# Kernel optimization log

Hardware: AMD Instinct MI355X
Metric: run time of the kernel (lower is better)

Reference implementation:

```python
import jax, jax.numpy as jnp
import numpy as np

DPITCH_RANGE = 24.0
SCALE = 1.0

B, T, ND, SD, H = 8192, 256, 8, 3, 64
HIST = 64
L = T - HIST  # generated LSTM steps; L+1 outputs emitted
IN = ND + SD + 1


def setup_inputs() -> dict:
    key = jax.random.key(0)
    ks = jax.random.split(key, 11)
    s = 1.0 / np.sqrt(H)

    def u(k, shape):
        return jax.random.uniform(k, shape, jnp.float32, -s, s)

    return {
        "noise": jax.random.normal(ks[0], (B, T, ND), jnp.float32),
        "hist_x": jax.random.normal(ks[1], (B, HIST, SD), jnp.float32) * 0.1,
        "gap_duration": jax.random.uniform(ks[2], (B, L + 1, SD - 1), jnp.float32),
        "W_ih": u(ks[3], (4 * H, IN)),
        "W_hh": u(ks[4], (4 * H, H)),
        "b_ih": u(ks[5], (4 * H,)),
        "b_hh": u(ks[6], (4 * H,)),
        "W1": u(ks[7], (H, H)),
        "b1": u(ks[8], (H,)),
        "W2": u(ks[9], (1, H)),
        "b2": u(ks[10], (1,)),
    }


def reference(noise, hist_x, gap_duration, W_ih, W_hh, b_ih, b_hh, W1, b1, W2, b2):
    hist_len = hist_x.shape[1]
    bias = b_ih + b_hh

    def lstm_cell(x, h, c):
        # PyTorch gate order: i, f, g, o
        gates = x @ W_ih.T + h @ W_hh.T + bias
        i, f, g, o = jnp.split(gates, 4, axis=-1)
        c = jax.nn.sigmoid(f) * c + jax.nn.sigmoid(i) * jnp.tanh(g)
        h = jax.nn.sigmoid(o) * jnp.tanh(c)
        return h, c

    # ---- conditioning on history ----
    dist = jnp.cumsum(hist_x[:, :, -1:], axis=1)                 # [B,HIST,1]
    cond_in = jnp.concatenate([hist_x, dist, noise[:, :hist_len]], axis=-1)  # [B,HIST,IN]
    h0 = jnp.zeros((noise.shape[0], W_hh.shape[1]), noise.dtype)
    c0 = jnp.zeros_like(h0)

    def cond_step(carry, x_t):
        h, c = carry
        h, c = lstm_cell(x_t, h, c)
        return (h, c), None

    (h, c), _ = jax.lax.scan(cond_step, (h0, c0), jnp.swapaxes(cond_in, 0, 1))
    output = h                      # last LSTM output [B,H]
    dist = dist[:, -1, :]           # [B,1]

    gen_noise = noise[:, hist_len:]                               # [B,L,ND]
    # pad one zero step: the final LSTM update is computed but unused
    gen_noise = jnp.concatenate(
        [gen_noise, jnp.zeros((gen_noise.shape[0], 1, gen_noise.shape[2]), gen_noise.dtype)], axis=1)
    xs = (jnp.swapaxes(gap_duration, 0, 1), jnp.swapaxes(gen_noise, 0, 1))

    def gen_step(carry, x_t):
        h, c, out, dist = carry
        gd, nz = x_t
        z = jnp.tanh(jnp.tanh(out @ W1.T + b1) @ W2.T + b2)       # output_net
        dp = z * DPITCH_RANGE * SCALE                             # [B,1]
        x = jnp.concatenate([gd, dp], axis=-1)                    # [B,SD]
        dist = dist + dp
        inp = jnp.concatenate([x, dist, nz], axis=-1)             # [B,IN]
        h, c = lstm_cell(inp, h, c)
        return (h, c, h, dist), x

    _, gen_xs = jax.lax.scan(gen_step, (h, c, output, dist), xs)  # [L+1,B,SD]
    output_seq = jnp.swapaxes(gen_xs, 0, 1)                       # [B,L+1,SD]
    return jnp.concatenate([hist_x, output_seq], axis=1)          # [B,HIST+L+1,SD]
```

## Files before the change

### kernel.cpp

```cpp
#include <hip/hip_runtime.h>
#include <stdint.h>

typedef unsigned short u16;
typedef unsigned int u32;
typedef __attribute__((ext_vector_type(8))) short short8v;
typedef __attribute__((ext_vector_type(4))) float f32x4;

#define NB 16
#define HISTN 64
#define TGEN 193

#define S_NOISE 2048
#define S_HIST  192
#define S_GAP   386
#define S_OUT   771

#define HROW 104
#define L2E  1.442695041f
#define L2E2 2.885390082f

__device__ __forceinline__ float b2f(u16 u) { return __uint_as_float(((u32)u) << 16); }
__device__ __forceinline__ u16 f2b(float f) {
    u32 u = __float_as_uint(f);
    u32 r = (u + 0x7fffu + ((u >> 16) & 1u)) >> 16;
    return (u16)r;
}
__device__ __forceinline__ float rcp_(float x) { return __builtin_amdgcn_rcpf(x); }
__device__ __forceinline__ float ex2(float x) { return __builtin_amdgcn_exp2f(x); }
__device__ __forceinline__ u32 cvtpk(float a, float b) {
    u32 r; asm("v_cvt_pk_bf16_f32 %0, %1, %2" : "=v"(r) : "v"(a), "v"(b)); return r;
}
__device__ __forceinline__ float tanh2(float s) {
    return __builtin_fmaf(-2.0f, rcp_(1.0f + ex2(s)), 1.0f);
}
__device__ __forceinline__ float cellh(const f32x4 a, float& c) {
    float iv = rcp_(1.0f + ex2(a[0]));
    float fv = rcp_(1.0f + ex2(a[1]));
    float gv = tanh2(a[2]);
    float ov = rcp_(1.0f + ex2(a[3]));
    c = __builtin_fmaf(fv, c, iv * gv);
    return ov * tanh2(L2E2 * c);
}
__device__ __forceinline__ float ldv(const void* p, int idx, bool f32) {
    return f32 ? ((const float*)p)[idx] : b2f(((const u16*)p)[idx]);
}
__device__ __forceinline__ void sync_lds() {
    asm volatile("s_waitcnt lgkmcnt(0)" ::: "memory");
    __builtin_amdgcn_s_barrier();
}

extern "C" __global__ void __launch_bounds__(512, 4)
lstm_gen_kernel(const void* __restrict__ noise, const void* __restrict__ hist_x,
                const void* __restrict__ gap, const void* __restrict__ pW_ih,
                const void* __restrict__ pW_hh, const void* __restrict__ pb_ih,
                const void* __restrict__ pb_hh, const void* __restrict__ pW1,
                const void* __restrict__ pb1, const void* __restrict__ pW2,
                const void* __restrict__ pb2, void* __restrict__ out)
{
    __shared__ u16 hb[2][NB * HROW];
    __shared__ u16 cxsA[HISTN][NB][8];
    __shared__ u16 cxsB[HISTN][NB][8];
    __shared__ u32 gdsb[TGEN * NB];
    __shared__ u16 nring[32][NB][8];
    __shared__ float zpl[NB * 4];
    __shared__ float dpd[NB];

    const int tid = threadIdx.x;
    const int lane = tid & 63;
    const int w = tid >> 6;
    const int lg = lane >> 4;
    const int ln = lane & 15;

    bool is_f32 = false;
    {
        const u32* p = (const u32*)pW_hh;
        for (int i = 0; i < 64; i++) {
            u32 v = p[i];
            float a = b2f((u16)(v & 0xffffu));
            float bb = b2f((u16)(v >> 16));
            if (!(fabsf(a) <= 0.5f) || !(fabsf(bb) <= 0.5f)) is_f32 = true;
        }
    }

    float* hs = (float*)gdsb;

    for (int i = tid; i < NB * HROW; i += 512) ((u32*)hb)[i] = 0u;
    for (int i = tid; i < HISTN * NB * 3; i += 512) {
        int t = i / 48, r = i % 48, b = r / 3, k = r % 3;
        hs[i] = ldv(hist_x, ((size_t)blockIdx.x * NB + b) * S_HIST + t * 3 + k, is_f32);
    }
    for (int i = tid; i < HISTN * NB * 4; i += 512) {
        int t = i >> 6, r = i & 63, b = r >> 2, q = r & 3;
        size_t base = ((size_t)blockIdx.x * NB + b) * S_NOISE + t * 8;
        u32 v;
        if (is_f32) {
            const float* p = (const float*)noise + base + q * 2;
            v = (u32)f2b(p[0]) | ((u32)f2b(p[1]) << 16);
        } else v = ((const u32*)noise)[(base >> 1) + q];
        ((u32*)&cxsB[t][b][0])[q] = v;
    }
    {
        const int s = tid >> 4, b = tid & 15;
        size_t base = ((size_t)blockIdx.x * NB + b) * S_NOISE + (size_t)(HISTN + s) * 8;
        u32 r0, r1, r2, r3;
        if (is_f32) {
            const float* nf = (const float*)noise + base;
            float4 a = *(const float4*)nf, bq = *(const float4*)(nf + 4);
            r0 = (u32)f2b(a.x) | ((u32)f2b(a.y) << 16);
            r1 = (u32)f2b(a.z) | ((u32)f2b(a.w) << 16);
            r2 = (u32)f2b(bq.x) | ((u32)f2b(bq.y) << 16);
            r3 = (u32)f2b(bq.z) | ((u32)f2b(bq.w) << 16);
        } else {
            uint4 nv = *(const uint4*)((const u16*)noise + base);
            r0 = nv.x; r1 = nv.y; r2 = nv.z; r3 = nv.w;
        }
        u32* dst = (u32*)&nring[s][b][0];
        dst[0] = r0; dst[1] = r1; dst[2] = r2; dst[3] = r3;
    }
    for (int i = tid; i < NB * HISTN * 3; i += 512) {
        int b = i / 192, e = i % 192;
        size_t bt = (size_t)blockIdx.x * NB + b;
        if (is_f32) ((float*)out)[bt * S_OUT + e] = ((const float*)hist_x)[bt * S_HIST + e];
        else ((u16*)out)[bt * S_OUT + e] = ((const u16*)hist_x)[bt * S_HIST + e];
    }
    __syncthreads();

    if (tid < NB) {
        float dd = 0.0f;
#pragma unroll 1
        for (int t = 0; t < HISTN; t++) {
            float x0 = hs[t * 48 + tid * 3 + 0];
            float x1 = hs[t * 48 + tid * 3 + 1];
            float x2 = hs[t * 48 + tid * 3 + 2];
            dd += x2;
            u16 dph = f2b(x2); u16 dpl = f2b(x2 - b2f(dph));
            u16 dsh = f2b(dd); u16 dsl = f2b(dd - b2f(dsh));
            u32* dst = (u32*)&cxsA[t][tid][0];
            dst[0] = (u32)f2b(x0) | ((u32)f2b(x1) << 16);
            dst[1] = (u32)dph | ((u32)dpl << 16);
            dst[2] = (u32)dsh | ((u32)dsl << 16);
            dst[3] = (u32)dsh | ((u32)dph << 16);
        }
        dpd[tid] = dd;
    }
    __syncthreads();

    for (int i = tid; i < TGEN * NB; i += 512) {
        int t = i >> 4, b = i & 15;
        size_t base = ((size_t)blockIdx.x * NB + b) * S_GAP + t * 2;
        u32 v;
        if (is_f32) {
            const float* p = (const float*)gap + base;
            v = (u32)f2b(p[0]) | ((u32)f2b(p[1]) << 16);
        } else v = *(const u32*)((const u16*)gap + base);
        gdsb[i] = v;
    }

    short8v a00, a01, a02, a10, a11, a12;
#pragma unroll
    for (int T = 0; T < 2; T++) {
        const int j = (T << 5) | (w << 2) | (ln >> 2);
        const int g = ln & 3;
        const int row = (g << 6) | j;
        const float rs = (g == 2) ? L2E2 : -L2E;
        float wdp = ldv(pW_ih, row * 12 + 2, is_f32) * rs;
        u16 wdph = f2b(wdp); u16 wdpl = f2b(wdp - b2f(wdph));
        float wds = ldv(pW_ih, row * 12 + 3, is_f32) * rs;
        u16 wdsh = f2b(wds); u16 wdsl = f2b(wds - b2f(wdsh));
        short8v f0, f1, f2;
#pragma unroll
        for (int e = 0; e < 8; e++) {
            const int c = lg * 8 + e;
            f0[e] = (short)f2b(ldv(pW_hh, row * 64 + c, is_f32) * rs);
            f1[e] = (short)f2b(ldv(pW_hh, row * 64 + 32 + c, is_f32) * rs);
            u16 v = 0;
            if (c == 0 || c == 1) v = f2b(ldv(pW_ih, row * 12 + c, is_f32) * rs);
            else if (c == 2 || c == 3) v = wdph;
            else if (c == 4 || c == 5) v = wdsh;
            else if (c == 6) v = wdsl;
            else if (c == 7) v = wdpl;
            else if (c >= 8 && c < 16) v = f2b(ldv(pW_ih, row * 12 + (c - 4), is_f32) * rs);
            f2[e] = (short)v;
        }
        if (T == 0) { a00 = f0; a01 = f1; a02 = f2; }
        else        { a10 = f0; a11 = f1; a12 = f2; }
    }

    f32x4 bias0, bias1, wd0, wd1, ws0, ws1;
#pragma unroll
    for (int T = 0; T < 2; T++) {
        const int jc = (T << 5) | (w << 2) | lg;
        f32x4 bv, dv, sv;
#pragma unroll
        for (int q = 0; q < 4; q++) {
            const int row = (q << 6) | jc;
            const float qs = (q == 2) ? L2E2 : -L2E;
            bv[q] = (ldv(pb_ih, row, is_f32) + ldv(pb_hh, row, is_f32)) * qs;
            dv[q] = ldv(pW_ih, row * 12 + 2, is_f32) * qs;
            sv[q] = ldv(pW_ih, row * 12 + 3, is_f32) * qs;
        }
        if (T == 0) { bias0 = bv; wd0 = dv; ws0 = sv; }
        else        { bias1 = bv; wd1 = dv; ws1 = sv; }
    }

    const bool mlpw = (w >= 4);
    short8v w1F0 = {}, w1F1 = {};
    f32x4 b1v = {0.f, 0.f, 0.f, 0.f};
    float w2L[4] = {0.f, 0.f, 0.f, 0.f};
    if (mlpw) {
        const int wp = w - 4;
        const int row1 = (wp << 4) | ln;
#pragma unroll
        for (int e = 0; e < 8; e++) {
            w1F0[e] = (short)f2b(ldv(pW1, row1 * 64 + lg * 8 + e, is_f32) * L2E2);
            w1F1[e] = (short)f2b(ldv(pW1, row1 * 64 + 32 + lg * 8 + e, is_f32) * L2E2);
        }
        const int rq = (wp << 4) | (lg << 2);
#pragma unroll
        for (int q = 0; q < 4; q++) {
            b1v[q] = ldv(pb1, rq + q, is_f32) * L2E2;
            w2L[q] = ldv(pW2, rq + q, is_f32) * L2E2;
        }
    }
    const float b2vs = ldv(pb2, 0, is_f32) * L2E2;

    const size_t gb = (size_t)blockIdx.x * NB + (size_t)ln;
    const float* gd_f = (const float*)gap + gb * S_GAP;
    u16* out_h = (u16*)out + gb * S_OUT;
    float* out_f = (float*)out + gb * S_OUT;

    float cst0 = 0.f, cst1 = 0.f;
    int pc = 0;
    __syncthreads();

#pragma unroll 1
    for (int t = 0; t < HISTN; t++) {
        const u16* hc = hb[pc];
        u16* hn = hb[pc ^ 1];
        short8v bf0 = *(const short8v*)&hc[ln * HROW + lg * 8];
        short8v bf1 = *(const short8v*)&hc[ln * HROW + 32 + lg * 8];
        short8v bf2 = {};
        if (lg == 0) bf2 = *(const short8v*)&cxsA[t][ln][0];
        else if (lg == 1) bf2 = *(const short8v*)&cxsB[t][ln][0];
        f32x4 acc0 = bias0, acc1 = bias1;
        acc0 = __builtin_amdgcn_mfma_f32_16x16x32_bf16(a00, bf0, acc0, 0, 0, 0);
        acc0 = __builtin_amdgcn_mfma_f32_16x16x32_bf16(a01, bf1, acc0, 0, 0, 0);
        acc0 = __builtin_amdgcn_mfma_f32_16x16x32_bf16(a02, bf2, acc0, 0, 0, 0);
        acc1 = __builtin_amdgcn_mfma_f32_16x16x32_bf16(a10, bf0, acc1, 0, 0, 0);
        acc1 = __builtin_amdgcn_mfma_f32_16x16x32_bf16(a11, bf1, acc1, 0, 0, 0);
        acc1 = __builtin_amdgcn_mfma_f32_16x16x32_bf16(a12, bf2, acc1, 0, 0, 0);
        float h0 = cellh(acc0, cst0);
        float h1 = cellh(acc1, cst1);
        u32 hp = cvtpk(h0, h1);
        const int j0 = (w << 2) | lg;
        hn[ln * HROW + j0] = (u16)hp;
        hn[ln * HROW + j0 + 32] = (u16)(hp >> 16);
        sync_lds();
        pc ^= 1;
    }

    float dist = dpd[ln];
    float gdf0 = 0.f, gdf1 = 0.f;
    if (is_f32 && tid < NB) { gdf0 = gd_f[0]; gdf1 = gd_f[1]; }

#pragma unroll 1
    for (int tg = 0; tg < TGEN; tg++) {
        u16* hB = hb[0];
        short8v bf0 = *(const short8v*)&hB[ln * HROW + lg * 8];
        short8v bf1 = *(const short8v*)&hB[ln * HROW + 32 + lg * 8];
        short8v bf2 = {};
        u32 g32 = 0;
        if (lg == 0) {
            g32 = gdsb[(tg << 4) | ln];
            bf2[0] = (short)(g32 & 0xffffu); bf2[1] = (short)(g32 >> 16);
        } else if (lg == 1) {
            union { uint4 u; short8v s; } cvt;
            cvt.u = *(const uint4*)&nring[tg & 31][ln][0];
            bf2 = cvt.s;
        }
        f32x4 acc0 = bias0, acc1 = bias1;
        acc0 = __builtin_amdgcn_mfma_f32_16x16x32_bf16(a00, bf0, acc0, 0, 0, 0);
        acc0 = __builtin_amdgcn_mfma_f32_16x16x32_bf16(a01, bf1, acc0, 0, 0, 0);
        acc0 = __builtin_amdgcn_mfma_f32_16x16x32_bf16(a02, bf2, acc0, 0, 0, 0);
        acc1 = __builtin_amdgcn_mfma_f32_16x16x32_bf16(a10, bf0, acc1, 0, 0, 0);
        acc1 = __builtin_amdgcn_mfma_f32_16x16x32_bf16(a11, bf1, acc1, 0, 0, 0);
        acc1 = __builtin_amdgcn_mfma_f32_16x16x32_bf16(a12, bf2, acc1, 0, 0, 0);
        if (mlpw) {
            f32x4 m0 = b1v;
            m0 = __builtin_amdgcn_mfma_f32_16x16x32_bf16(w1F0, bf0, m0, 0, 0, 0);
            m0 = __builtin_amdgcn_mfma_f32_16x16x32_bf16(w1F1, bf1, m0, 0, 0, 0);
            float mp = w2L[0] * tanh2(m0[0]) + w2L[1] * tanh2(m0[1])
                     + w2L[2] * tanh2(m0[2]) + w2L[3] * tanh2(m0[3]);
            mp += __shfl_xor(mp, 16);
            mp += __shfl_xor(mp, 32);
            if (lg == 0) zpl[(ln << 2) | (w - 4)] = mp;
        }
        if (((tg & 15) == 0) && tg > 0 && tg <= 176 && tid < 256) {
            const int s = tid >> 4, b = tid & 15;
            const int t = HISTN + tg + 16 + s;
            u32 r0 = 0, r1 = 0, r2 = 0, r3 = 0;
            if (t < 256) {
                size_t base = ((size_t)blockIdx.x * NB + b) * S_NOISE + (size_t)t * 8;
                if (is_f32) {
                    const float* nf = (const float*)noise + base;
                    float4 a = *(const float4*)nf, bq = *(const float4*)(nf + 4);
                    r0 = (u32)f2b(a.x) | ((u32)f2b(a.y) << 16);
                    r1 = (u32)f2b(a.z) | ((u32)f2b(a.w) << 16);
                    r2 = (u32)f2b(bq.x) | ((u32)f2b(bq.y) << 16);
                    r3 = (u32)f2b(bq.z) | ((u32)f2b(bq.w) << 16);
                } else {
                    uint4 nv = *(const uint4*)((const u16*)noise + base);
                    r0 = nv.x; r1 = nv.y; r2 = nv.z; r3 = nv.w;
                }
            }
            u32* dst = (u32*)&nring[(tg + 16 + s) & 31][b][0];
            dst[0] = r0; dst[1] = r1; dst[2] = r2; dst[3] = r3;
        }
        sync_lds();
        f32x4 zr = *(const f32x4*)&zpl[ln << 2];
        float th = tanh2(b2vs + zr[0] + zr[1] + zr[2] + zr[3]);
        float dp = 24.0f * th;
        dist += dp;
#pragma unroll
        for (int q = 0; q < 4; q++) {
            acc0[q] += wd0[q] * dp + ws0[q] * dist;
            acc1[q] += wd1[q] * dp + ws1[q] * dist;
        }
        float h0 = cellh(acc0, cst0);
        float h1 = cellh(acc1, cst1);
        u32 hp = cvtpk(h0, h1);
        const int j0 = (w << 2) | lg;
        hB[ln * HROW + j0] = (u16)hp;
        hB[ln * HROW + j0 + 32] = (u16)(hp >> 16);
        if (tid < NB) {
            const int to = HISTN + tg;
            if (is_f32) {
                out_f[to * 3] = gdf0; out_f[to * 3 + 1] = gdf1; out_f[to * 3 + 2] = dp;
                if (tg + 1 < TGEN) { gdf0 = gd_f[(tg + 1) * 2]; gdf1 = gd_f[(tg + 1) * 2 + 1]; }
            } else {
                out_h[to * 3] = (u16)(g32 & 0xffffu);
                out_h[to * 3 + 1] = (u16)(g32 >> 16);
                out_h[to * 3 + 2] = f2b(dp);
            }
        }
        sync_lds();
    }
}

extern "C" void kernel_launch(void* const* d_in, const int* in_sizes, int n_in,
                              void* d_out, int out_size, void* d_ws, size_t ws_size,
                              hipStream_t stream) {
    (void)in_sizes; (void)n_in; (void)d_ws; (void)ws_size; (void)out_size;
    lstm_gen_kernel<<<512, 512, 0, stream>>>(
        d_in[0], d_in[1], d_in[2], d_in[3], d_in[4], d_in[5],
        d_in[6], d_in[7], d_in[8], d_in[9], d_in[10], d_out);
}
```

Baseline: 435.8 us.

## Interleave hidden units per lane and merge input buffers into unified LDS rows

Each lane's two hidden units become adjacent (u = w*8 + lg*2 + T), so the packed bf16 pair is written with one 32-bit LDS store instead of two 16-bit stores. The separate cond-phase input buffers and the gap/noise buffers are merged into single 16-element-per-batch rows, so the extra MFMA operand is one 16-byte LDS load instead of branchy partial loads. Gap values now stream through the same 32-slot ring as noise instead of being staged in full, which shrinks LDS use. The dp/dist correction is also written as explicit FMAs.

```diff
diff --git a/kernel.cpp b/kernel.cpp
--- a/kernel.cpp
+++ b/kernel.cpp
@@ -58,10 +58,8 @@
                 const void* __restrict__ pb2, void* __restrict__ out)
 {
     __shared__ u16 hb[2][NB * HROW];
-    __shared__ u16 cxsA[HISTN][NB][8];
-    __shared__ u16 cxsB[HISTN][NB][8];
-    __shared__ u32 gdsb[TGEN * NB];
-    __shared__ u16 nring[32][NB][8];
+    __shared__ u16 cxs[HISTN][NB][16];
+    __shared__ u16 xr[32][NB][16];
     __shared__ float zpl[NB * 4];
     __shared__ float dpd[NB];
 
@@ -82,7 +80,7 @@
         }
     }
 
-    float* hs = (float*)gdsb;
+    float* hs = (float*)xr;
 
     for (int i = tid; i < NB * HROW; i += 512) ((u32*)hb)[i] = 0u;
     for (int i = tid; i < HISTN * NB * 3; i += 512) {
@@ -97,25 +95,7 @@
             const float* p = (const float*)noise + base + q * 2;
             v = (u32)f2b(p[0]) | ((u32)f2b(p[1]) << 16);
         } else v = ((const u32*)noise)[(base >> 1) + q];
-        ((u32*)&cxsB[t][b][0])[q] = v;
-    }
-    {
-        const int s = tid >> 4, b = tid & 15;
-        size_t base = ((size_t)blockIdx.x * NB + b) * S_NOISE + (size_t)(HISTN + s) * 8;
-        u32 r0, r1, r2, r3;
-        if (is_f32) {
-            const float* nf = (const float*)noise + base;
-            float4 a = *(const float4*)nf, bq = *(const float4*)(nf + 4);
-            r0 = (u32)f2b(a.x) | ((u32)f2b(a.y) << 16);
-            r1 = (u32)f2b(a.z) | ((u32)f2b(a.w) << 16);
-            r2 = (u32)f2b(bq.x) | ((u32)f2b(bq.y) << 16);
-            r3 = (u32)f2b(bq.z) | ((u32)f2b(bq.w) << 16);
-        } else {
-            uint4 nv = *(const uint4*)((const u16*)noise + base);
-            r0 = nv.x; r1 = nv.y; r2 = nv.z; r3 = nv.w;
-        }
-        u32* dst = (u32*)&nring[s][b][0];
-        dst[0] = r0; dst[1] = r1; dst[2] = r2; dst[3] = r3;
+        ((u32*)&cxs[t][b][8])[q] = v;
     }
     for (int i = tid; i < NB * HISTN * 3; i += 512) {
         int b = i / 192, e = i % 192;
@@ -135,7 +115,7 @@
             dd += x2;
             u16 dph = f2b(x2); u16 dpl = f2b(x2 - b2f(dph));
             u16 dsh = f2b(dd); u16 dsl = f2b(dd - b2f(dsh));
-            u32* dst = (u32*)&cxsA[t][tid][0];
+            u32* dst = (u32*)&cxs[t][tid][0];
             dst[0] = (u32)f2b(x0) | ((u32)f2b(x1) << 16);
             dst[1] = (u32)dph | ((u32)dpl << 16);
             dst[2] = (u32)dsh | ((u32)dsl << 16);
@@ -145,23 +125,38 @@
     }
     __syncthreads();
 
-    for (int i = tid; i < TGEN * NB; i += 512) {
-        int t = i >> 4, b = i & 15;
-        size_t base = ((size_t)blockIdx.x * NB + b) * S_GAP + t * 2;
-        u32 v;
+    {
+        const int s = tid >> 4, b = tid & 15;
+        u32* row = (u32*)&xr[s][b][0];
+        size_t gbase = ((size_t)blockIdx.x * NB + b) * S_GAP + s * 2;
+        u32 gv;
         if (is_f32) {
-            const float* p = (const float*)gap + base;
-            v = (u32)f2b(p[0]) | ((u32)f2b(p[1]) << 16);
-        } else v = *(const u32*)((const u16*)gap + base);
-        gdsb[i] = v;
+            const float* p = (const float*)gap + gbase;
+            gv = (u32)f2b(p[0]) | ((u32)f2b(p[1]) << 16);
+        } else gv = *(const u32*)((const u16*)gap + gbase);
+        row[0] = gv; row[1] = 0u; row[2] = 0u; row[3] = 0u;
+        size_t nbase = ((size_t)blockIdx.x * NB + b) * S_NOISE + (size_t)(HISTN + s) * 8;
+        u32 r0, r1, r2, r3;
+        if (is_f32) {
+            const float* nf = (const float*)noise + nbase;
+            float4 a = *(const float4*)nf, bq = *(const float4*)(nf + 4);
+            r0 = (u32)f2b(a.x) | ((u32)f2b(a.y) << 16);
+            r1 = (u32)f2b(a.z) | ((u32)f2b(a.w) << 16);
+            r2 = (u32)f2b(bq.x) | ((u32)f2b(bq.y) << 16);
+            r3 = (u32)f2b(bq.z) | ((u32)f2b(bq.w) << 16);
+        } else {
+            uint4 nv = *(const uint4*)((const u16*)noise + nbase);
+            r0 = nv.x; r1 = nv.y; r2 = nv.z; r3 = nv.w;
+        }
+        row[4] = r0; row[5] = r1; row[6] = r2; row[7] = r3;
     }
 
     short8v a00, a01, a02, a10, a11, a12;
 #pragma unroll
     for (int T = 0; T < 2; T++) {
-        const int j = (T << 5) | (w << 2) | (ln >> 2);
+        const int u = (w << 3) | ((ln >> 2) << 1) | T;
         const int g = ln & 3;
-        const int row = (g << 6) | j;
+        const int row = (g << 6) | u;
         const float rs = (g == 2) ? L2E2 : -L2E;
         float wdp = ldv(pW_ih, row * 12 + 2, is_f32) * rs;
         u16 wdph = f2b(wdp); u16 wdpl = f2b(wdp - b2f(wdph));
@@ -189,11 +184,11 @@
     f32x4 bias0, bias1, wd0, wd1, ws0, ws1;
 #pragma unroll
     for (int T = 0; T < 2; T++) {
-        const int jc = (T << 5) | (w << 2) | lg;
+        const int u = (w << 3) | (lg << 1) | T;
         f32x4 bv, dv, sv;
 #pragma unroll
         for (int q = 0; q < 4; q++) {
-            const int row = (q << 6) | jc;
+            const int row = (q << 6) | u;
             const float qs = (q == 2) ? L2E2 : -L2E;
             bv[q] = (ldv(pb_ih, row, is_f32) + ldv(pb_hh, row, is_f32)) * qs;
             dv[q] = ldv(pW_ih, row * 12 + 2, is_f32) * qs;
@@ -231,6 +226,7 @@
 
     float cst0 = 0.f, cst1 = 0.f;
     int pc = 0;
+    const int hoff = (w << 3) | (lg << 1);
     __syncthreads();
 
 #pragma unroll 1
@@ -240,8 +236,7 @@
         short8v bf0 = *(const short8v*)&hc[ln * HROW + lg * 8];
         short8v bf1 = *(const short8v*)&hc[ln * HROW + 32 + lg * 8];
         short8v bf2 = {};
-        if (lg == 0) bf2 = *(const short8v*)&cxsA[t][ln][0];
-        else if (lg == 1) bf2 = *(const short8v*)&cxsB[t][ln][0];
+        if (lg < 2) bf2 = *(const short8v*)&cxs[t][ln][lg * 8];
         f32x4 acc0 = bias0, acc1 = bias1;
         acc0 = __builtin_amdgcn_mfma_f32_16x16x32_bf16(a00, bf0, acc0, 0, 0, 0);
         acc0 = __builtin_amdgcn_mfma_f32_16x16x32_bf16(a01, bf1, acc0, 0, 0, 0);
@@ -251,10 +246,7 @@
         acc1 = __builtin_amdgcn_mfma_f32_16x16x32_bf16(a12, bf2, acc1, 0, 0, 0);
         float h0 = cellh(acc0, cst0);
         float h1 = cellh(acc1, cst1);
-        u32 hp = cvtpk(h0, h1);
-        const int j0 = (w << 2) | lg;
-        hn[ln * HROW + j0] = (u16)hp;
-        hn[ln * HROW + j0 + 32] = (u16)(hp >> 16);
+        *(u32*)&hn[ln * HROW + hoff] = cvtpk(h0, h1);
         sync_lds();
         pc ^= 1;
     }
@@ -269,15 +261,7 @@
         short8v bf0 = *(const short8v*)&hB[ln * HROW + lg * 8];
         short8v bf1 = *(const short8v*)&hB[ln * HROW + 32 + lg * 8];
         short8v bf2 = {};
-        u32 g32 = 0;
-        if (lg == 0) {
-            g32 = gdsb[(tg << 4) | ln];
-            bf2[0] = (short)(g32 & 0xffffu); bf2[1] = (short)(g32 >> 16);
-        } else if (lg == 1) {
-            union { uint4 u; short8v s; } cvt;
-            cvt.u = *(const uint4*)&nring[tg & 31][ln][0];
-            bf2 = cvt.s;
-        }
+        if (lg < 2) bf2 = *(const short8v*)&xr[tg & 31][ln][lg * 8];
         f32x4 acc0 = bias0, acc1 = bias1;
         acc0 = __builtin_amdgcn_mfma_f32_16x16x32_bf16(a00, bf0, acc0, 0, 0, 0);
         acc0 = __builtin_amdgcn_mfma_f32_16x16x32_bf16(a01, bf1, acc0, 0, 0, 0);
@@ -297,24 +281,33 @@
         }
         if (((tg & 15) == 0) && tg > 0 && tg <= 176 && tid < 256) {
             const int s = tid >> 4, b = tid & 15;
-            const int t = HISTN + tg + 16 + s;
+            const int tga = tg + 16 + s;
+            u32* row = (u32*)&xr[tga & 31][b][0];
+            u32 gv = 0;
+            if (tga < TGEN) {
+                size_t gbase = ((size_t)blockIdx.x * NB + b) * S_GAP + tga * 2;
+                if (is_f32) {
+                    const float* p = (const float*)gap + gbase;
+                    gv = (u32)f2b(p[0]) | ((u32)f2b(p[1]) << 16);
+                } else gv = *(const u32*)((const u16*)gap + gbase);
+            }
+            row[0] = gv;
             u32 r0 = 0, r1 = 0, r2 = 0, r3 = 0;
-            if (t < 256) {
-                size_t base = ((size_t)blockIdx.x * NB + b) * S_NOISE + (size_t)t * 8;
+            if (HISTN + tga < 256) {
+                size_t nbase = ((size_t)blockIdx.x * NB + b) * S_NOISE + (size_t)(HISTN + tga) * 8;
                 if (is_f32) {
-                    const float* nf = (const float*)noise + base;
+                    const float* nf = (const float*)noise + nbase;
                     float4 a = *(const float4*)nf, bq = *(const float4*)(nf + 4);
                     r0 = (u32)f2b(a.x) | ((u32)f2b(a.y) << 16);
                     r1 = (u32)f2b(a.z) | ((u32)f2b(a.w) << 16);
                     r2 = (u32)f2b(bq.x) | ((u32)f2b(bq.y) << 16);
                     r3 = (u32)f2b(bq.z) | ((u32)f2b(bq.w) << 16);
                 } else {
-                    uint4 nv = *(const uint4*)((const u16*)noise + base);
+                    uint4 nv = *(const uint4*)((const u16*)noise + nbase);
                     r0 = nv.x; r1 = nv.y; r2 = nv.z; r3 = nv.w;
                 }
             }
-            u32* dst = (u32*)&nring[(tg + 16 + s) & 31][b][0];
-            dst[0] = r0; dst[1] = r1; dst[2] = r2; dst[3] = r3;
+            row[4] = r0; row[5] = r1; row[6] = r2; row[7] = r3;
         }
         sync_lds();
         f32x4 zr = *(const f32x4*)&zpl[ln << 2];
@@ -323,21 +316,19 @@
         dist += dp;
 #pragma unroll
         for (int q = 0; q < 4; q++) {
-            acc0[q] += wd0[q] * dp + ws0[q] * dist;
-            acc1[q] += wd1[q] * dp + ws1[q] * dist;
+            acc0[q] = __builtin_fmaf(wd0[q], dp, __builtin_fmaf(ws0[q], dist, acc0[q]));
+            acc1[q] = __builtin_fmaf(wd1[q], dp, __builtin_fmaf(ws1[q], dist, acc1[q]));
         }
         float h0 = cellh(acc0, cst0);
         float h1 = cellh(acc1, cst1);
-        u32 hp = cvtpk(h0, h1);
-        const int j0 = (w << 2) | lg;
-        hB[ln * HROW + j0] = (u16)hp;
-        hB[ln * HROW + j0 + 32] = (u16)(hp >> 16);
+        *(u32*)&hB[ln * HROW + hoff] = cvtpk(h0, h1);
         if (tid < NB) {
             const int to = HISTN + tg;
             if (is_f32) {
                 out_f[to * 3] = gdf0; out_f[to * 3 + 1] = gdf1; out_f[to * 3 + 2] = dp;
                 if (tg + 1 < TGEN) { gdf0 = gd_f[(tg + 1) * 2]; gdf1 = gd_f[(tg + 1) * 2 + 1]; }
             } else {
+                u32 g32 = *(const u32*)&xr[tg & 31][ln][0];
                 out_h[to * 3] = (u16)(g32 & 0xffffu);
                 out_h[to * 3 + 1] = (u16)(g32 >> 16);
                 out_h[to * 3 + 2] = f2b(dp);
```

After: 424.9 us. 2.5% less time.
